# Kernel tuning notes

Hardware: AMD Instinct MI355X
Metric: run time of the kernel (lower is better)

Reference implementation:

```python
import jax, jax.numpy as jnp
import numpy as np

N = 25000      # nodes
E = 400000     # directed edges (avg degree 16)
F_IN = 133     # atom feature dim (QM_137k)
H = 8          # heads
C = 64         # hidden per head
HC = H * C     # 512
OUT = 1
NEG_SLOPE = 0.2
BN_EPS = 1e-5


def setup_inputs() -> dict:
    key = jax.random.key(0)
    ks = jax.random.split(key, 8)
    s = 0.05
    return {
        "x": jax.random.normal(ks[0], (N, F_IN), jnp.float32),
        "edge_index": jax.random.randint(ks[1], (2, E), 0, N, dtype=jnp.int32),
        # GATv2Conv params (share_weights=False): W_l for src, W_r for dst, att vector per head
        "Wl": jax.random.normal(ks[2], (F_IN, HC), jnp.float32) * s,
        "Wr": jax.random.normal(ks[3], (F_IN, HC), jnp.float32) * s,
        "att": jax.random.normal(ks[4], (H, C), jnp.float32) * s,
        "b1": jnp.zeros((HC,), jnp.float32),
        # BatchNorm1d (eval mode: running stats)
        "bn_gamma": jnp.ones((HC,), jnp.float32),
        "bn_beta": jnp.zeros((HC,), jnp.float32),
        "bn_mean": jnp.zeros((HC,), jnp.float32),
        "bn_var": jnp.ones((HC,), jnp.float32),
        # PReLU (default: single shared weight, init 0.25)
        "prelu_w": jnp.full((1,), 0.25, jnp.float32),
        # GCNConv params
        "Wg": jax.random.normal(ks[5], (HC, OUT), jnp.float32) * s,
        "bg": jnp.zeros((OUT,), jnp.float32),
    }


def _with_self_loops(edge_index):
    loops = jnp.arange(N, dtype=edge_index.dtype)
    src = jnp.concatenate([edge_index[0], loops])
    dst = jnp.concatenate([edge_index[1], loops])
    return src, dst


def _gatv2(x, edge_index, Wl, Wr, att, b1):
    # PyG GATv2Conv, concat=True, add_self_loops=True, eval (attention dropout off)
    src, dst = _with_self_loops(edge_index)
    xl = (x @ Wl).reshape(N, H, C)   # source-side transform
    xr = (x @ Wr).reshape(N, H, C)   # target-side transform
    msg = xl[src]                    # [E', H, C] gathered source messages
    e = jnp.einsum('ehc,hc->eh', jax.nn.leaky_relu(msg + xr[dst], NEG_SLOPE), att)  # [E', H]
    # segment softmax over incoming edges of each dst node (self loops => no empty segments)
    emax = jax.ops.segment_max(e, dst, num_segments=N)
    ee = jnp.exp(e - emax[dst])
    den = jax.ops.segment_sum(ee, dst, num_segments=N)
    agg = jax.ops.segment_sum(ee[:, :, None] * msg, dst, num_segments=N)  # [N, H, C]
    out = agg / den[:, :, None]
    return out.reshape(N, HC) + b1


def _gcn(x, edge_index, Wg, bg):
    # PyG GCNConv: add self loops, sym-normalized aggregation of x @ W, plus bias
    src, dst = _with_self_loops(edge_index)
    deg = jax.ops.segment_sum(jnp.ones_like(dst, dtype=x.dtype), dst, num_segments=N)
    dinv = jax.lax.rsqrt(jnp.maximum(deg, 1.0))
    h = x @ Wg                                   # [N, OUT]
    norm = dinv[src] * dinv[dst]                 # [E']
    return jax.ops.segment_sum(norm[:, None] * h[src], dst, num_segments=N) + bg


def reference(x, edge_index, Wl, Wr, att, b1, bn_gamma, bn_beta, bn_mean, bn_var,
              prelu_w, Wg, bg):
    h = _gatv2(x, edge_index, Wl, Wr, att, b1)
    # BatchNorm1d (eval) + PReLU
    h = (h - bn_mean) * jax.lax.rsqrt(bn_var + BN_EPS) * bn_gamma + bn_beta
    h = jnp.where(h >= 0, h, prelu_w * h)
    # dropout is identity in eval mode
    out = _gcn(h, edge_index, Wg, bg)
    return out.squeeze()  # [N]
```

## Files before the change

### kernel.cpp

```cpp
#include <hip/hip_runtime.h>

#define NN 25000
#define EE 400000
#define FIN 133
#define HCC 512
#define RPAD 25088
#define KPAD 160
#define NT 5
#define CAP 64
#define EPB 4082

typedef __attribute__((ext_vector_type(8))) __bf16 bf16x8;
typedef __attribute__((ext_vector_type(4))) float f32x4;
typedef __attribute__((ext_vector_type(8))) _Float16 f16x8;
typedef __attribute__((ext_vector_type(2))) _Float16 f16x2;

static __device__ __forceinline__ ushort f2bf(float f) {
    uint32_t u = __float_as_uint(f);
    uint32_t r = (u + 0x7fffu + ((u >> 16) & 1u)) >> 16;
    return (ushort)r;
}
static __device__ __forceinline__ float bf2f(ushort b) {
    return __uint_as_float(((uint32_t)b) << 16);
}

static __device__ __forceinline__ f16x2 lrelu2(f16x2 t) {
#if __has_builtin(__builtin_elementwise_max) && __has_builtin(__builtin_elementwise_min)
    const f16x2 z = {(_Float16)0.f, (_Float16)0.f};
    const f16x2 c = {(_Float16)0.2f, (_Float16)0.2f};
    return __builtin_elementwise_min(t, z) * c + __builtin_elementwise_max(t, z);
#else
    f16x2 r;
    r[0] = t[0] >= (_Float16)0.f ? t[0] : (_Float16)((float)t[0] * 0.2f);
    r[1] = t[1] >= (_Float16)0.f ? t[1] : (_Float16)((float)t[1] * 0.2f);
    return r;
#endif
}
static __device__ __forceinline__ float fdot2f(f16x2 a, f16x2 b, float c) {
#if __has_builtin(__builtin_amdgcn_fdot2)
    return __builtin_amdgcn_fdot2(a, b, c, false);
#else
    return c + (float)a[0] * (float)b[0] + (float)a[1] * (float)b[1];
#endif
}

__global__ __launch_bounds__(256) void k_prep(const float* __restrict__ x,
    const float* __restrict__ Wl, const float* __restrict__ Wr,
    ushort* __restrict__ ah, ushort* __restrict__ al,
    ushort* __restrict__ wh, ushort* __restrict__ wl)
{
    const int tid = threadIdx.x;
    const int y = blockIdx.y;
    if (y < 20) {
        const int row = blockIdx.x * 256 + tid;
        const int oct = y;
        const int kb = oct * 8;
        ushort h[8], l[8];
        #pragma unroll
        for (int j = 0; j < 8; ++j) {
            int k = kb + j;
            float v = (row < NN && k < FIN) ? x[(size_t)row * FIN + k] : 0.f;
            ushort hh = f2bf(v);
            h[j] = hh;
            l[j] = f2bf(v - bf2f(hh));
        }
        uint4 H, L;
        H.x = h[0] | (h[1] << 16); H.y = h[2] | (h[3] << 16);
        H.z = h[4] | (h[5] << 16); H.w = h[6] | (h[7] << 16);
        L.x = l[0] | (l[1] << 16); L.y = l[2] | (l[3] << 16);
        L.z = l[4] | (l[5] << 16); L.w = l[6] | (l[7] << 16);
        size_t slot = (size_t)oct * RPAD + row;
        ((uint4*)ah)[slot] = H;
        ((uint4*)al)[slot] = L;
    } else {
        if (blockIdx.x >= 80) return;
        const int oct = blockIdx.x >> 2;
        const int col = (blockIdx.x & 3) * 256 + tid;
        const int kb = oct * 8;
        const float* W = (col < 512) ? Wl : Wr;
        const int c = (col < 512) ? col : col - 512;
        ushort h[8], l[8];
        #pragma unroll
        for (int j = 0; j < 8; ++j) {
            int k = kb + j;
            float v = (k < FIN) ? W[(size_t)k * 512 + c] : 0.f;
            ushort hh = f2bf(v);
            h[j] = hh;
            l[j] = f2bf(v - bf2f(hh));
        }
        uint4 H, L;
        H.x = h[0] | (h[1] << 16); H.y = h[2] | (h[3] << 16);
        H.z = h[4] | (h[5] << 16); H.w = h[6] | (h[7] << 16);
        L.x = l[0] | (l[1] << 16); L.y = l[2] | (l[3] << 16);
        L.z = l[4] | (l[5] << 16); L.w = l[6] | (l[7] << 16);
        size_t slot = (size_t)oct * 1024 + col;
        ((uint4*)wh)[slot] = H;
        ((uint4*)wl)[slot] = L;
    }
}

__global__ __launch_bounds__(256, 3) void k_gemm3(
    const ushort* __restrict__ ah, const ushort* __restrict__ al,
    const ushort* __restrict__ wh, const ushort* __restrict__ wl,
    ushort* __restrict__ xl, ushort* __restrict__ xr,
    const int* __restrict__ srcp, const int* __restrict__ dstp,
    int* __restrict__ cnt, int* __restrict__ csr)
{
    if (blockIdx.y >= 196) {
        int sbid = (blockIdx.y - 196) * 8 + blockIdx.x;
        if (sbid < 98) {
            int e0 = sbid * EPB;
            int e1 = e0 + EPB; if (e1 > EE) e1 = EE;
            for (int e = e0 + threadIdx.x; e < e1; e += 256) {
                int d = dstp[e];
                int pos = atomicAdd(&cnt[d], 1);
                csr[d * CAP + pos] = srcp[e];
            }
        }
        return;
    }
    const int tid = threadIdx.x;
    const int wid = tid >> 6, lane = tid & 63;
    const int row0 = blockIdx.y * 128;
    const int cb = blockIdx.x * 128;
    const bool isR = cb >= 512;
    const int oc0 = isR ? cb - 512 : cb;
    const int wr = wid >> 1, wc = wid & 1;
    const int kg = lane >> 4, r = lane & 15;

    const int arow = row0 + wr * 64 + r;
    const int bcol = cb + wc * 64 + r;

    f32x4 acc[4][4];
    #pragma unroll
    for (int i = 0; i < 4; ++i)
        #pragma unroll
        for (int j = 0; j < 4; ++j) acc[i][j] = (f32x4)0.f;

    #pragma unroll
    for (int t = 0; t < NT; ++t) {
        const size_t abase = (size_t)(t * 4 + kg) * RPAD + arow;
        const size_t bbase = (size_t)(t * 4 + kg) * 1024 + bcol;
        bf16x8 fah[4], fal[4], fbh[4], fbl[4];
        #pragma unroll
        for (int i = 0; i < 4; ++i) {
            fah[i] = ((const bf16x8*)ah)[abase + i * 16];
            fal[i] = ((const bf16x8*)al)[abase + i * 16];
            fbh[i] = ((const bf16x8*)wh)[bbase + i * 16];
            fbl[i] = ((const bf16x8*)wl)[bbase + i * 16];
        }
        #pragma unroll
        for (int i = 0; i < 4; ++i)
            #pragma unroll
            for (int j = 0; j < 4; ++j)
                acc[i][j] = __builtin_amdgcn_mfma_f32_16x16x32_bf16(fah[i], fbh[j], acc[i][j], 0, 0, 0);
        #pragma unroll
        for (int i = 0; i < 4; ++i)
            #pragma unroll
            for (int j = 0; j < 4; ++j)
                acc[i][j] = __builtin_amdgcn_mfma_f32_16x16x32_bf16(fah[i], fbl[j], acc[i][j], 0, 0, 0);
        #pragma unroll
        for (int i = 0; i < 4; ++i)
            #pragma unroll
            for (int j = 0; j < 4; ++j)
                acc[i][j] = __builtin_amdgcn_mfma_f32_16x16x32_bf16(fal[i], fbh[j], acc[i][j], 0, 0, 0);
    }
    ushort* __restrict__ outp = isR ? xr : xl;
    const int cl = lane & 15, rq = lane >> 4;
    #pragma unroll
    for (int i = 0; i < 4; ++i) {
        #pragma unroll
        for (int rr = 0; rr < 4; ++rr) {
            int row = row0 + wr * 64 + i * 16 + rq * 4 + rr;
            if (row < NN) {
                #pragma unroll
                for (int j = 0; j < 4; ++j) {
                    _Float16 hv = (_Float16)acc[i][j][rr];
                    outp[(size_t)row * HCC + oc0 + wc * 64 + j * 16 + cl] =
                        *(const ushort*)&hv;
                }
            }
        }
    }
}

__global__ __launch_bounds__(256) void k_gat(
    const ushort* __restrict__ xl, const ushort* __restrict__ xr,
    const float* __restrict__ att, const float* __restrict__ b1,
    const float* __restrict__ gam, const float* __restrict__ bet,
    const float* __restrict__ mean, const float* __restrict__ var,
    const float* __restrict__ pw, const float* __restrict__ Wg,
    const int* __restrict__ cnt, const int* __restrict__ csr,
    float* __restrict__ g, float* __restrict__ dinvp)
{
    const int lane = threadIdx.x & 63;
    const int node = blockIdx.x * 4 + (threadIdx.x >> 6);
    const int sb = lane * 8;
    f16x8 xv = *(const f16x8*)&xr[(size_t)node * HCC + sb];
    float4 a0 = *(const float4*)&att[sb];
    float4 a1 = *(const float4*)&att[sb + 4];
    f16x2 xrh[4], avh[4];
    {
        const f16x2* xp = (const f16x2*)&xv;
        xrh[0] = xp[0]; xrh[1] = xp[1]; xrh[2] = xp[2]; xrh[3] = xp[3];
    }
    avh[0] = {(_Float16)a0.x, (_Float16)a0.y};
    avh[1] = {(_Float16)a0.z, (_Float16)a0.w};
    avh[2] = {(_Float16)a1.x, (_Float16)a1.y};
    avh[3] = {(_Float16)a1.z, (_Float16)a1.w};
    float s = 0.f;
    float acc[8] = {0.f, 0.f, 0.f, 0.f, 0.f, 0.f, 0.f, 0.f};
    const int deg = cnt[node];
    const int beg = node * CAP;
    auto process = [&](f16x8 hv) {
        const f16x2* hp = (const f16x2*)&hv;
        float ep = 0.f;
        #pragma unroll
        for (int p = 0; p < 4; ++p) {
            f16x2 t = hp[p] + xrh[p];
            ep = fdot2f(lrelu2(t), avh[p], ep);
        }
        ep += __shfl_xor(ep, 1);
        ep += __shfl_xor(ep, 2);
        ep += __shfl_xor(ep, 4);
        float w = __expf(ep);
        s += w;
        const _Float16* he = (const _Float16*)&hv;
        #pragma unroll
        for (int k = 0; k < 8; ++k) acc[k] += w * (float)he[k];
    };
    auto row = [&](int srcn) -> f16x8 {
        return *(const f16x8*)&xl[(size_t)srcn * HCC + sb];
    };
    process(row(node));
    int j = 0;
    for (; j + 4 <= deg; j += 4) {
        int sA = csr[beg + j], sB = csr[beg + j + 1];
        int sC = csr[beg + j + 2], sD = csr[beg + j + 3];
        f16x8 hA = row(sA);
        f16x8 hB = row(sB);
        f16x8 hC = row(sC);
        f16x8 hD = row(sD);
        process(hA); process(hB); process(hC); process(hD);
    }
    for (; j < deg; ++j) process(row(csr[beg + j]));
    float inv = 1.f / s;
    float p_w = pw[0];
    float dot = 0.f;
    #pragma unroll
    for (int k = 0; k < 8; ++k) {
        int idx = sb + k;
        float v = acc[k] * inv + b1[idx];
        v = (v - mean[idx]) * rsqrtf(var[idx] + 1e-5f) * gam[idx] + bet[idx];
        v = v >= 0.f ? v : p_w * v;
        dot += v * Wg[idx];
    }
    dot += __shfl_xor(dot, 1);
    dot += __shfl_xor(dot, 2);
    dot += __shfl_xor(dot, 4);
    dot += __shfl_xor(dot, 8);
    dot += __shfl_xor(dot, 16);
    dot += __shfl_xor(dot, 32);
    if (lane == 0) {
        float dn = rsqrtf((float)(deg + 1));
        g[node] = dn * dot;
        dinvp[node] = dn;
    }
}

__global__ __launch_bounds__(256) void k_gcn(
    const float* __restrict__ g, const float* __restrict__ dinv,
    const int* __restrict__ cnt, const int* __restrict__ csr,
    const float* __restrict__ bg, float* __restrict__ out)
{
    int t = blockIdx.x * 256 + threadIdx.x;
    int node = t >> 2;
    int sub = t & 3;
    if (node >= NN) return;
    int deg = cnt[node];
    int base = node * CAP;
    float s = 0.f;
    for (int j = sub; j < deg; j += 4) s += g[csr[base + j]];
    s += __shfl_xor(s, 1);
    s += __shfl_xor(s, 2);
    if (sub == 0) out[node] = dinv[node] * (g[node] + s) + bg[0];
}

extern "C" void kernel_launch(void* const* d_in, const int* in_sizes, int n_in,
                              void* d_out, int out_size, void* d_ws, size_t ws_size,
                              hipStream_t stream)
{
    const float* x    = (const float*)d_in[0];
    const int*   ei   = (const int*)d_in[1];
    const float* Wl   = (const float*)d_in[2];
    const float* Wr   = (const float*)d_in[3];
    const float* att  = (const float*)d_in[4];
    const float* b1   = (const float*)d_in[5];
    const float* gam  = (const float*)d_in[6];
    const float* bet  = (const float*)d_in[7];
    const float* mean = (const float*)d_in[8];
    const float* var  = (const float*)d_in[9];
    const float* pw   = (const float*)d_in[10];
    const float* Wg   = (const float*)d_in[11];
    const float* bg   = (const float*)d_in[12];
    float* out = (float*)d_out;

    char* base = (char*)d_ws;
    size_t o = 0;
    ushort* xl  = (ushort*)(base + o); o += (size_t)NN * HCC * 2;
    ushort* xr  = (ushort*)(base + o); o += (size_t)NN * HCC * 2;
    o = (o + 15) & ~(size_t)15;
    float* g    = (float*)(base + o); o += NN * 4;
    float* dinv = (float*)(base + o); o += NN * 4;
    int*   cnt  = (int*)(base + o);   o += NN * 4;
    int*   csr  = (int*)(base + o);   o += (size_t)NN * CAP * 4;
    o = (o + 15) & ~(size_t)15;
    ushort* ah = (ushort*)(base + o); o += (size_t)RPAD * KPAD * 2;
    ushort* al = (ushort*)(base + o); o += (size_t)RPAD * KPAD * 2;
    ushort* wh = (ushort*)(base + o); o += (size_t)KPAD * 1024 * 2;
    ushort* wl = (ushort*)(base + o); o += (size_t)KPAD * 1024 * 2;

    const int* srcp = ei;
    const int* dstp = ei + EE;

    hipMemsetAsync(cnt, 0, NN * sizeof(int), stream);
    k_prep<<<dim3(98, 21), 256, 0, stream>>>(x, Wl, Wr, ah, al, wh, wl);
    k_gemm3<<<dim3(8, 209), 256, 0, stream>>>(ah, al, wh, wl, xl, xr,
                                              srcp, dstp, cnt, csr);
    k_gat<<<NN / 4, 256, 0, stream>>>(xl, xr, att, b1, gam, bet, mean, var, pw, Wg,
                                      cnt, csr, g, dinv);
    k_gcn<<<(NN * 4 + 255) / 256, 256, 0, stream>>>(g, dinv, cnt, csr, bg, out);
}
```

Baseline: 220.8 us.

## Move CSR build into prep kernel and double-buffer GEMM fragment loads

The edge-bucketing work (atomic count plus CSR fill) moves out of the GEMM kernel into extra blocks of the prep kernel, so the GEMM grid holds only compute tiles. The GEMM K loop now prefetches the next K-slice's bf16 fragments into a second register buffer while the MFMAs for the current slice run, and the launch_bounds occupancy hint of 3 is dropped. The aim is to hide global-load latency behind MFMA work and keep atomic-heavy blocks from sharing the GEMM launch. The cost is much higher register pressure, which may reduce occupancy or cause spills.

```diff
diff --git a/kernel.cpp b/kernel.cpp
--- a/kernel.cpp
+++ b/kernel.cpp
@@ -47,10 +47,22 @@
 __global__ __launch_bounds__(256) void k_prep(const float* __restrict__ x,
     const float* __restrict__ Wl, const float* __restrict__ Wr,
     ushort* __restrict__ ah, ushort* __restrict__ al,
-    ushort* __restrict__ wh, ushort* __restrict__ wl)
+    ushort* __restrict__ wh, ushort* __restrict__ wl,
+    const int* __restrict__ srcp, const int* __restrict__ dstp,
+    int* __restrict__ cnt, int* __restrict__ csr)
 {
     const int tid = threadIdx.x;
     const int y = blockIdx.y;
+    if (y == 21) {
+        int e0 = blockIdx.x * EPB;
+        int e1 = e0 + EPB; if (e1 > EE) e1 = EE;
+        for (int e = e0 + tid; e < e1; e += 256) {
+            int d = dstp[e];
+            int pos = atomicAdd(&cnt[d], 1);
+            csr[d * CAP + pos] = srcp[e];
+        }
+        return;
+    }
     if (y < 20) {
         const int row = blockIdx.x * 256 + tid;
         const int oct = y;
@@ -99,26 +111,11 @@
     }
 }
 
-__global__ __launch_bounds__(256, 3) void k_gemm3(
+__global__ __launch_bounds__(256) void k_gemm3(
     const ushort* __restrict__ ah, const ushort* __restrict__ al,
     const ushort* __restrict__ wh, const ushort* __restrict__ wl,
-    ushort* __restrict__ xl, ushort* __restrict__ xr,
-    const int* __restrict__ srcp, const int* __restrict__ dstp,
-    int* __restrict__ cnt, int* __restrict__ csr)
-{
-    if (blockIdx.y >= 196) {
-        int sbid = (blockIdx.y - 196) * 8 + blockIdx.x;
-        if (sbid < 98) {
-            int e0 = sbid * EPB;
-            int e1 = e0 + EPB; if (e1 > EE) e1 = EE;
-            for (int e = e0 + threadIdx.x; e < e1; e += 256) {
-                int d = dstp[e];
-                int pos = atomicAdd(&cnt[d], 1);
-                csr[d * CAP + pos] = srcp[e];
-            }
-        }
-        return;
-    }
+    ushort* __restrict__ xl, ushort* __restrict__ xr)
+{
     const int tid = threadIdx.x;
     const int wid = tid >> 6, lane = tid & 63;
     const int row0 = blockIdx.y * 128;
@@ -137,33 +134,45 @@
         #pragma unroll
         for (int j = 0; j < 4; ++j) acc[i][j] = (f32x4)0.f;
 
+    bf16x8 cah[2][4], cal[2][4], cbh[2][4], cbl[2][4];
+    #pragma unroll
+    for (int i = 0; i < 4; ++i) {
+        const size_t abase = (size_t)kg * RPAD + arow;
+        const size_t bbase = (size_t)kg * 1024 + bcol;
+        cah[0][i] = ((const bf16x8*)ah)[abase + i * 16];
+        cal[0][i] = ((const bf16x8*)al)[abase + i * 16];
+        cbh[0][i] = ((const bf16x8*)wh)[bbase + i * 16];
+        cbl[0][i] = ((const bf16x8*)wl)[bbase + i * 16];
+    }
     #pragma unroll
     for (int t = 0; t < NT; ++t) {
-        const size_t abase = (size_t)(t * 4 + kg) * RPAD + arow;
-        const size_t bbase = (size_t)(t * 4 + kg) * 1024 + bcol;
-        bf16x8 fah[4], fal[4], fbh[4], fbl[4];
-        #pragma unroll
-        for (int i = 0; i < 4; ++i) {
-            fah[i] = ((const bf16x8*)ah)[abase + i * 16];
-            fal[i] = ((const bf16x8*)al)[abase + i * 16];
-            fbh[i] = ((const bf16x8*)wh)[bbase + i * 16];
-            fbl[i] = ((const bf16x8*)wl)[bbase + i * 16];
+        const int cur = t & 1, nxt = cur ^ 1;
+        if (t + 1 < NT) {
+            const size_t abase = (size_t)((t + 1) * 4 + kg) * RPAD + arow;
+            const size_t bbase = (size_t)((t + 1) * 4 + kg) * 1024 + bcol;
+            #pragma unroll
+            for (int i = 0; i < 4; ++i) {
+                cah[nxt][i] = ((const bf16x8*)ah)[abase + i * 16];
+                cal[nxt][i] = ((const bf16x8*)al)[abase + i * 16];
+                cbh[nxt][i] = ((const bf16x8*)wh)[bbase + i * 16];
+                cbl[nxt][i] = ((const bf16x8*)wl)[bbase + i * 16];
+            }
         }
         #pragma unroll
         for (int i = 0; i < 4; ++i)
             #pragma unroll
             for (int j = 0; j < 4; ++j)
-                acc[i][j] = __builtin_amdgcn_mfma_f32_16x16x32_bf16(fah[i], fbh[j], acc[i][j], 0, 0, 0);
+                acc[i][j] = __builtin_amdgcn_mfma_f32_16x16x32_bf16(cah[cur][i], cbh[cur][j], acc[i][j], 0, 0, 0);
         #pragma unroll
         for (int i = 0; i < 4; ++i)
             #pragma unroll
             for (int j = 0; j < 4; ++j)
-                acc[i][j] = __builtin_amdgcn_mfma_f32_16x16x32_bf16(fah[i], fbl[j], acc[i][j], 0, 0, 0);
+                acc[i][j] = __builtin_amdgcn_mfma_f32_16x16x32_bf16(cah[cur][i], cbl[cur][j], acc[i][j], 0, 0, 0);
         #pragma unroll
         for (int i = 0; i < 4; ++i)
             #pragma unroll
             for (int j = 0; j < 4; ++j)
-                acc[i][j] = __builtin_amdgcn_mfma_f32_16x16x32_bf16(fal[i], fbh[j], acc[i][j], 0, 0, 0);
+                acc[i][j] = __builtin_amdgcn_mfma_f32_16x16x32_bf16(cal[cur][i], cbh[cur][j], acc[i][j], 0, 0, 0);
     }
     ushort* __restrict__ outp = isR ? xr : xl;
     const int cl = lane & 15, rq = lane >> 4;
@@ -324,9 +333,9 @@
     const int* dstp = ei + EE;
 
     hipMemsetAsync(cnt, 0, NN * sizeof(int), stream);
-    k_prep<<<dim3(98, 21), 256, 0, stream>>>(x, Wl, Wr, ah, al, wh, wl);
-    k_gemm3<<<dim3(8, 209), 256, 0, stream>>>(ah, al, wh, wl, xl, xr,
-                                              srcp, dstp, cnt, csr);
+    k_prep<<<dim3(98, 22), 256, 0, stream>>>(x, Wl, Wr, ah, al, wh, wl,
+                                             srcp, dstp, cnt, csr);
+    k_gemm3<<<dim3(8, 196), 256, 0, stream>>>(ah, al, wh, wl, xl, xr);
     k_gat<<<NN / 4, 256, 0, stream>>>(xl, xr, att, b1, gam, bet, mean, var, pw, Wg,
                                       cnt, csr, g, dinv);
     k_gcn<<<(NN * 4 + 255) / 256, 256, 0, stream>>>(g, dinv, cnt, csr, bg, out);
```

After: 229.0 us. 1.04x slower.
